# Performance work log

Measured on AMD Instinct MI355X. Metric: run time of the kernel, lower is better.

Reference implementation:

```python
import jax, jax.numpy as jnp
import numpy as np
from jax import lax

S, B, V, D, H, L, C = 2048, 32, 50000, 512, 512, 2, 10


def setup_inputs() -> dict:
    key = jax.random.key(0)
    ks = jax.random.split(key, 6)
    x = jax.random.randint(ks[0], (S, B), 0, V)  # (seq, batch) token ids
    embed = jax.random.normal(ks[1], (V, D), jnp.float32) * 0.1
    # per layer: W maps input -> [x_tilde, f_gate, r_gate], each H wide
    W = jax.random.normal(ks[2], (L, D, 3 * H), jnp.float32) * (1.0 / np.sqrt(D))
    b = jnp.zeros((L, 2 * H), jnp.float32)  # biases for f and r gates
    Wc = jax.random.normal(ks[3], (H, C), jnp.float32) * 0.05
    bc = jnp.zeros((C,), jnp.float32)
    return {"x": x, "embed": embed, "W": W, "b": b, "Wc": Wc, "bc": bc}


def _sru_layer(h_in, W_l, b_l):
    # h_in: (S, B, H) (input dim == hidden dim -> identity highway skip)
    U = jnp.einsum('sbd,dk->sbk', h_in, W_l)  # (S, B, 3H)
    xt, fg, rg = jnp.split(U, 3, axis=-1)
    bf, br = jnp.split(b_l, 2)
    f = jax.nn.sigmoid(fg + bf)
    r = jax.nn.sigmoid(rg + br)

    def step(c, inp):
        f_t, xt_t = inp
        c = f_t * c + (1.0 - f_t) * xt_t  # elementwise light recurrence
        return c, c

    c0 = jnp.zeros((h_in.shape[1], f.shape[-1]), h_in.dtype)
    _, cs = lax.scan(step, c0, (f, xt))  # cs: (S, B, H)
    # highway output
    return r * jnp.tanh(cs) + (1.0 - r) * h_in


def reference(x, embed, W, b, Wc, bc):
    h = embed[x]  # (S, B, D); dropout layers are identity at inference
    for l in range(W.shape[0]):
        h = _sru_layer(h, W[l], b[l])
    out = jnp.tanh(h)            # (S, B, H)
    pooled = jnp.max(out, axis=0)  # max-pool over time -> (B, H)
    pooled = jnp.tanh(pooled)
    return pooled @ Wc + bc      # (B, C)
```

## Files before the change

kernel.cpp:

```cpp
#include <hip/hip_runtime.h>
#include <cmath>

#define S_LEN 2048
#define B_SZ 32
#define D_DIM 512
#define H_DIM 512
#define C_NUM 10
#define M_ROWS (S_LEN * B_SZ)
#define BH (B_SZ * H_DIM)
#define N_COLS (3 * H_DIM)

#define SC 1024
#define SCH 32
#define NSUB 32
#define CROWS (SC * B_SZ)

typedef __bf16 bf16_t;
typedef bf16_t bf16x8 __attribute__((ext_vector_type(8)));
typedef float f32x4 __attribute__((ext_vector_type(4)));
typedef unsigned short ushort_t;

__device__ __forceinline__ unsigned int f2bf(float f) {
  union { float f; unsigned int u; } a;
  a.f = f;
  unsigned int r = a.u + 0x7FFFu + ((a.u >> 16) & 1u);
  return r >> 16;
}
__device__ __forceinline__ unsigned int pack2bf(float lo, float hi) {
  return f2bf(lo) | (f2bf(hi) << 16);
}
__device__ __forceinline__ float bflo(unsigned int u) {
  union { unsigned int u; float f; } a; a.u = u << 16; return a.f;
}
__device__ __forceinline__ float bfhi(unsigned int u) {
  union { unsigned int u; float f; } a; a.u = u & 0xffff0000u; return a.f;
}
__device__ __forceinline__ float sigf(float x) {
  return 1.f / (1.f + __expf(-x));
}
__device__ __forceinline__ float tanh_fast(float c) {
  float e = __expf(2.f * c);
  return 1.f - 2.f / (e + 1.f);
}
__device__ __forceinline__ void load16_lds(const void* g, void* l) {
  __builtin_amdgcn_global_load_lds(
      (const __attribute__((address_space(1))) unsigned int*)g,
      (__attribute__((address_space(3))) unsigned int*)l, 16, 0, 0);
}


__global__ __launch_bounds__(256) void gather_kernel(const int* __restrict__ x,
                                                     const float* __restrict__ embed,
                                                     uint4* __restrict__ E4) {
  int i = blockIdx.x * blockDim.x + threadIdx.x;
  const int total = M_ROWS * 16;
  int stride = gridDim.x * blockDim.x;
  for (; i < total; i += stride) {
    int m = i >> 4;
    int kg = (i & 15) * 4;
    int tile = m >> 7, row = m & 127;
    int xm = x[m];
    const float4* src = (const float4*)(embed + (size_t)xm * 512 + kg * 8);
    float4 v[8];
#pragma unroll
    for (int j = 0; j < 8; j++) v[j] = src[j];
    uint4* dst = E4 + (size_t)tile * 8192 + row;
#pragma unroll
    for (int j = 0; j < 4; j++) {
      dst[(size_t)(kg + j) * 128] =
          make_uint4(pack2bf(v[2 * j].x, v[2 * j].y), pack2bf(v[2 * j].z, v[2 * j].w),
                     pack2bf(v[2 * j + 1].x, v[2 * j + 1].y),
                     pack2bf(v[2 * j + 1].z, v[2 * j + 1].w));
    }
  }
}

__global__ __launch_bounds__(256) void wt_kernel(const float* __restrict__ W,
                                                 ushort_t* __restrict__ Wt) {
  int e = blockIdx.x * blockDim.x + threadIdx.x;
  if (e >= 2 * 786432) return;
  int l = e / 786432;
  int t = e - l * 786432;
  int ntile = t >> 16;
  int rr = t & 65535;
  int kc = rr >> 10;
  int row = (rr >> 3) & 127;
  int kk = t & 7;
  int n = ntile * 128 + row;
  int k = kc * 8 + kk;
  Wt[e] = (ushort_t)f2bf(W[(size_t)l * D_DIM * N_COLS + (size_t)k * N_COLS + n]);
}

__global__ __launch_bounds__(256, 3) void sru_gemm_bf16(
    const ushort_t* __restrict__ At,
    int tile0,
    const ushort_t* __restrict__ Bt,
    ushort_t* __restrict__ xt_out, ushort_t* __restrict__ f_out,
    ushort_t* __restrict__ r_out) {
  __shared__ ushort_t As[2][4096];
  __shared__ ushort_t Bs[2][4096];
  const int t = threadIdx.x;
  const int wave = t >> 6, lane = t & 63;
  const int cpx = gridDim.x >> 3;
  const int swz = (blockIdx.x & 7) * cpx + (blockIdx.x >> 3);
  const int nb = swz % 12, mb = swz / 12;
  const int m0 = mb * 128, n0 = nb * 128;
  const int wm = wave & 1, wn = wave >> 1;
  const int lrow = lane >> 4, lcol = lane & 15;

  f32x4 acc[4][4];
#pragma unroll
  for (int i = 0; i < 4; i++)
#pragma unroll
    for (int j = 0; j < 4; j++) acc[i][j] = (f32x4){0.f, 0.f, 0.f, 0.f};

  const ushort_t* Ab = At + ((size_t)(tile0 + mb) << 16);
  const ushort_t* Bb = Bt + ((size_t)nb << 16);
  const int c0 = wave * 2;
  const int le = lane * 8;

#define STAGE(buf, k0)                                                      \
  do {                                                                      \
    load16_lds(Ab + (k0) * 128 + (c0 + 0) * 512 + le, &As[buf][(c0 + 0) * 512]); \
    load16_lds(Ab + (k0) * 128 + (c0 + 1) * 512 + le, &As[buf][(c0 + 1) * 512]); \
    load16_lds(Bb + (k0) * 128 + (c0 + 0) * 512 + le, &Bs[buf][(c0 + 0) * 512]); \
    load16_lds(Bb + (k0) * 128 + (c0 + 1) * 512 + le, &Bs[buf][(c0 + 1) * 512]); \
  } while (0)

  STAGE(0, 0);
  __syncthreads();
  int cur = 0;
  for (int step = 0; step < 16; ++step) {
    if (step + 1 < 16) STAGE(cur ^ 1, (step + 1) * 32);
    bf16x8 af[4], bfr[4];
#pragma unroll
    for (int mi = 0; mi < 4; mi++)
      af[mi] = *reinterpret_cast<const bf16x8*>(
          &As[cur][(lrow * 128 + wm * 64 + mi * 16 + lcol) * 8]);
#pragma unroll
    for (int ni = 0; ni < 4; ni++)
      bfr[ni] = *reinterpret_cast<const bf16x8*>(
          &Bs[cur][(lrow * 128 + wn * 64 + ni * 16 + lcol) * 8]);
#pragma unroll
    for (int mi = 0; mi < 4; mi++)
#pragma unroll
      for (int ni = 0; ni < 4; ni++)
        acc[mi][ni] = __builtin_amdgcn_mfma_f32_16x16x32_bf16(
            bfr[ni], af[mi], acc[mi][ni], 0, 0, 0);
    __syncthreads();
    cur ^= 1;
  }
#undef STAGE

  const int region = n0 >> 9;
  ushort_t* outp = region == 0 ? xt_out : (region == 1 ? f_out : r_out);
  const int nloc0 = (n0 & 511) + wn * 64 + lrow * 4;
#pragma unroll
  for (int mi = 0; mi < 4; mi++) {
    const int m = m0 + wm * 64 + mi * 16 + lcol;
    const size_t mpart = ((size_t)(m >> 7) << 16) + ((size_t)(m & 127) << 3);
#pragma unroll
    for (int ni = 0; ni < 4; ni++) {
      const int nloc = nloc0 + ni * 16;
      size_t ad = mpart + ((size_t)(nloc >> 3) << 10) + (nloc & 7);
      uint2 pk;
      pk.x = pack2bf(acc[mi][ni][0], acc[mi][ni][1]);
      pk.y = pack2bf(acc[mi][ni][2], acc[mi][ni][3]);
      *(uint2*)&outp[ad] = pk;
    }
  }
}

template <int LAST>
__global__ __launch_bounds__(256) void scan_fused(
    const ushort_t* __restrict__ f, const ushort_t* __restrict__ xt,
    const ushort_t* __restrict__ r, const ushort_t* __restrict__ hw,
    ushort_t* __restrict__ ob, const float* __restrict__ bl,
    float* __restrict__ cstate, float* __restrict__ pmax,
    int first, int m0abs) {
  __shared__ float sA[8][32][8];
  __shared__ float sB[8][32][8];
  __shared__ float sC[8][32][8];
  const int tid = threadIdx.x;
  const int q = tid & 7, ch = tid >> 3;
  const int p = blockIdx.x * 8 + q;
  const int hc = p >> 5, b = p & 31;
  const int h0 = hc << 3;
  float bf_[8];
#pragma unroll
  for (int j = 0; j < 8; j++) bf_[j] = bl[h0 + j];

  {
    float Aa[8], Bv[8];
#pragma unroll
    for (int j = 0; j < 8; j++) { Aa[j] = 1.f; Bv[j] = 0.f; }
    for (int s = 0; s < SCH; s++) {
      int ml = ((ch * SCH + s) << 5) + b;
      size_t ga = ((size_t)(ml >> 7) << 16) + ((size_t)hc << 10) + ((ml & 127) << 3);
      uint4 fq = *(const uint4*)&f[ga];
      uint4 xq = *(const uint4*)&xt[ga];
      unsigned int fw[4] = {fq.x, fq.y, fq.z, fq.w};
      unsigned int xw[4] = {xq.x, xq.y, xq.z, xq.w};
#pragma unroll
      for (int w = 0; w < 4; w++) {
        float fa = sigf(bflo(fw[w]) + bf_[2 * w]);
        float fb = sigf(bfhi(fw[w]) + bf_[2 * w + 1]);
        Bv[2 * w]     = fa * Bv[2 * w]     + (1.f - fa) * bflo(xw[w]);
        Bv[2 * w + 1] = fb * Bv[2 * w + 1] + (1.f - fb) * bfhi(xw[w]);
        Aa[2 * w] *= fa;
        Aa[2 * w + 1] *= fb;
      }
    }
#pragma unroll
    for (int j = 0; j < 8; j++) { sA[j][ch][q] = Aa[j]; sB[j][ch][q] = Bv[j]; }
  }
  __syncthreads();

  if (tid < 64) {
    int qq = tid & 7, jj = tid >> 3;
    int pp = blockIdx.x * 8 + qq;
    int bb = pp & 31, hh = (pp >> 5) * 8 + jj;
    float c = first ? 0.f : cstate[bb * 512 + hh];
    float a_[NSUB], b_[NSUB];
#pragma unroll
    for (int cc = 0; cc < NSUB; cc++) { a_[cc] = sA[jj][cc][qq]; b_[cc] = sB[jj][cc][qq]; }
#pragma unroll
    for (int cc = 0; cc < NSUB; cc++) {
      sC[jj][cc][qq] = c;
      c = a_[cc] * c + b_[cc];
    }
    cstate[bb * 512 + hh] = c;
  }
  __syncthreads();

  float br_[8];
#pragma unroll
  for (int j = 0; j < 8; j++) br_[j] = bl[512 + h0 + j];
  float c[8], pm[8];
#pragma unroll
  for (int j = 0; j < 8; j++) { c[j] = sC[j][ch][q]; pm[j] = -1e30f; }
  for (int s = 0; s < SCH; s++) {
    int ml = ((ch * SCH + s) << 5) + b;
    size_t ga = ((size_t)(ml >> 7) << 16) + ((size_t)hc << 10) + ((ml & 127) << 3);
    int ma = m0abs + ml;
    size_t ha = ((size_t)(ma >> 7) << 16) + ((size_t)hc << 10) + ((ma & 127) << 3);
    uint4 fq = *(const uint4*)&f[ga];
    uint4 xq = *(const uint4*)&xt[ga];
    uint4 rq = *(const uint4*)&r[ga];
    uint4 hq = *(const uint4*)&hw[ha];
    unsigned int fw[4] = {fq.x, fq.y, fq.z, fq.w};
    unsigned int xw[4] = {xq.x, xq.y, xq.z, xq.w};
    unsigned int rw[4] = {rq.x, rq.y, rq.z, rq.w};
    unsigned int hv[4] = {hq.x, hq.y, hq.z, hq.w};
    unsigned int ow[4];
#pragma unroll
    for (int w = 0; w < 4; w++) {
      float fa = sigf(bflo(fw[w]) + bf_[2 * w]);
      float fb = sigf(bfhi(fw[w]) + bf_[2 * w + 1]);
      float ra = sigf(bflo(rw[w]) + br_[2 * w]);
      float rb = sigf(bfhi(rw[w]) + br_[2 * w + 1]);
      c[2 * w]     = fa * c[2 * w]     + (1.f - fa) * bflo(xw[w]);
      c[2 * w + 1] = fb * c[2 * w + 1] + (1.f - fb) * bfhi(xw[w]);
      float oa = ra * tanh_fast(c[2 * w]) + (1.f - ra) * bflo(hv[w]);
      float obv = rb * tanh_fast(c[2 * w + 1]) + (1.f - rb) * bfhi(hv[w]);
      if (LAST) {
        pm[2 * w] = fmaxf(pm[2 * w], oa);
        pm[2 * w + 1] = fmaxf(pm[2 * w + 1], obv);
      } else {
        ow[w] = pack2bf(oa, obv);
      }
    }
    if (!LAST) *(uint4*)&ob[ha] = make_uint4(ow[0], ow[1], ow[2], ow[3]);
  }
  if (LAST) {
    int lin = ch * BH + b * 512 + h0;
    if (first) {
#pragma unroll
      for (int j = 0; j < 8; j++) pmax[lin + j] = pm[j];
    } else {
#pragma unroll
      for (int j = 0; j < 8; j++) pmax[lin + j] = fmaxf(pmax[lin + j], pm[j]);
    }
  }
}

__global__ void pool_kernel(const float* __restrict__ pmax, float* __restrict__ pooled) {
  int rem = blockIdx.x * blockDim.x + threadIdx.x;
  float m = -1e30f;
  for (int ch = 0; ch < NSUB; ch++) m = fmaxf(m, pmax[ch * BH + rem]);
  pooled[rem] = tanhf(tanhf(m));
}

__global__ void out_gemm(const float* __restrict__ pooled, const float* __restrict__ Wc,
                         const float* __restrict__ bc, float* __restrict__ out) {
  __shared__ float pt[H_DIM];
  int b = blockIdx.x;
  for (int i = threadIdx.x; i < H_DIM; i += blockDim.x) pt[i] = pooled[b * H_DIM + i];
  __syncthreads();
  if (threadIdx.x < C_NUM) {
    int c = threadIdx.x;
    float acc = bc[c];
    for (int hh = 0; hh < H_DIM; hh++) acc = fmaf(pt[hh], Wc[hh * C_NUM + c], acc);
    out[b * C_NUM + c] = acc;
  }
}

extern "C" void kernel_launch(void* const* d_in, const int* in_sizes, int n_in,
                              void* d_out, int out_size, void* d_ws, size_t ws_size,
                              hipStream_t stream) {
  const int* x = (const int*)d_in[0];
  const float* embed = (const float*)d_in[1];
  const float* W = (const float*)d_in[2];
  const float* b = (const float*)d_in[3];
  const float* Wc = (const float*)d_in[4];
  const float* bc = (const float*)d_in[5];
  float* out = (float*)d_out;

  const size_t SZ_HB = (size_t)M_ROWS * H_DIM * 2;
  const size_t SZ_G  = (size_t)CROWS * H_DIM * 2;
  const size_t SZ_WT = 2ull * N_COLS * D_DIM * 2;
  const size_t SZ_BHf = (size_t)BH * 4;

  char* p = (char*)d_ws;
  float* cstate0 = (float*)p; p += SZ_BHf;
  float* cstate1 = (float*)p; p += SZ_BHf;
  float* pooled  = (float*)p; p += SZ_BHf;
  float* pmax    = (float*)p; p += (size_t)NSUB * SZ_BHf;
  ushort_t* Wt   = (ushort_t*)p; p += SZ_WT;
  ushort_t* E    = (ushort_t*)p; p += SZ_HB;
  ushort_t* OB   = (ushort_t*)p; p += SZ_HB;
  ushort_t* X0   = (ushort_t*)p; p += SZ_G;
  ushort_t* F0   = (ushort_t*)p; p += SZ_G;
  ushort_t* R0   = (ushort_t*)p;

  gather_kernel<<<4096, 256, 0, stream>>>(x, embed, (uint4*)E);
  wt_kernel<<<6144, 256, 0, stream>>>(W, Wt);

  const int gemm_blocks = (CROWS / 128) * (N_COLS / 128);
  const int NOUTER = S_LEN / SC;
  const float* bl0 = b;
  const float* bl1 = b + 2 * H_DIM;
  const ushort_t* Wt0 = Wt;
  const ushort_t* Wt1 = Wt + (size_t)N_COLS * D_DIM;

  for (int ci = 0; ci < NOUTER; ci++) {
    const int m0abs = ci * CROWS;
    const int tile0 = m0abs >> 7;
    sru_gemm_bf16<<<gemm_blocks, 256, 0, stream>>>(E, tile0, Wt0, X0, F0, R0);
    scan_fused<0><<<256, 256, 0, stream>>>(F0, X0, R0, E, OB, bl0, cstate0,
                                           nullptr, ci == 0, m0abs);
    sru_gemm_bf16<<<gemm_blocks, 256, 0, stream>>>(OB, tile0, Wt1, X0, F0, R0);
    scan_fused<1><<<256, 256, 0, stream>>>(F0, X0, R0, OB, nullptr, bl1, cstate1,
                                           pmax, ci == 0, m0abs);
  }

  pool_kernel<<<BH / 256, 256, 0, stream>>>(pmax, pooled);
  out_gemm<<<B_SZ, 256, 0, stream>>>(pooled, Wc, bc, out);
}
```

Baseline: 577.9 us.

## Triple-buffer GEMM LDS pipeline and widen scan to 1024-thread blocks

```diff
diff --git a/kernel.cpp b/kernel.cpp
--- a/kernel.cpp
+++ b/kernel.cpp
@@ -11,8 +11,8 @@
 #define N_COLS (3 * H_DIM)
 
 #define SC 1024
-#define SCH 32
-#define NSUB 32
+#define SCH 8
+#define NSUB 128
 #define CROWS (SC * B_SZ)
 
 typedef __bf16 bf16_t;
@@ -97,8 +97,8 @@
     const ushort_t* __restrict__ Bt,
     ushort_t* __restrict__ xt_out, ushort_t* __restrict__ f_out,
     ushort_t* __restrict__ r_out) {
-  __shared__ ushort_t As[2][4096];
-  __shared__ ushort_t Bs[2][4096];
+  __shared__ ushort_t As[3][4096];
+  __shared__ ushort_t Bs[3][4096];
   const int t = threadIdx.x;
   const int wave = t >> 6, lane = t & 63;
   const int cpx = gridDim.x >> 3;
@@ -128,10 +128,17 @@
   } while (0)
 
   STAGE(0, 0);
-  __syncthreads();
-  int cur = 0;
+  STAGE(1, 32);
+#pragma unroll
   for (int step = 0; step < 16; ++step) {
-    if (step + 1 < 16) STAGE(cur ^ 1, (step + 1) * 32);
+    if (step < 15)
+      asm volatile("s_waitcnt vmcnt(4)" ::: "memory");
+    else
+      asm volatile("s_waitcnt vmcnt(0)" ::: "memory");
+    __builtin_amdgcn_s_barrier();
+    asm volatile("" ::: "memory");
+    if (step < 14) STAGE((step + 2) % 3, (step + 2) * 32);
+    const int cur = step % 3;
     bf16x8 af[4], bfr[4];
 #pragma unroll
     for (int mi = 0; mi < 4; mi++)
@@ -147,8 +154,6 @@
       for (int ni = 0; ni < 4; ni++)
         acc[mi][ni] = __builtin_amdgcn_mfma_f32_16x16x32_bf16(
             bfr[ni], af[mi], acc[mi][ni], 0, 0, 0);
-    __syncthreads();
-    cur ^= 1;
   }
 #undef STAGE
 
@@ -172,15 +177,14 @@
 }
 
 template <int LAST>
-__global__ __launch_bounds__(256) void scan_fused(
+__global__ __launch_bounds__(1024) void scan_fused(
     const ushort_t* __restrict__ f, const ushort_t* __restrict__ xt,
     const ushort_t* __restrict__ r, const ushort_t* __restrict__ hw,
     ushort_t* __restrict__ ob, const float* __restrict__ bl,
     float* __restrict__ cstate, float* __restrict__ pmax,
     int first, int m0abs) {
-  __shared__ float sA[8][32][8];
-  __shared__ float sB[8][32][8];
-  __shared__ float sC[8][32][8];
+  __shared__ float sA[8][NSUB][8];
+  __shared__ float sB[8][NSUB][8];
   const int tid = threadIdx.x;
   const int q = tid & 7, ch = tid >> 3;
   const int p = blockIdx.x * 8 + q;
@@ -221,13 +225,11 @@
     int pp = blockIdx.x * 8 + qq;
     int bb = pp & 31, hh = (pp >> 5) * 8 + jj;
     float c = first ? 0.f : cstate[bb * 512 + hh];
-    float a_[NSUB], b_[NSUB];
-#pragma unroll
-    for (int cc = 0; cc < NSUB; cc++) { a_[cc] = sA[jj][cc][qq]; b_[cc] = sB[jj][cc][qq]; }
-#pragma unroll
     for (int cc = 0; cc < NSUB; cc++) {
-      sC[jj][cc][qq] = c;
-      c = a_[cc] * c + b_[cc];
+      float a = sA[jj][cc][qq];
+      float bv = sB[jj][cc][qq];
+      sA[jj][cc][qq] = c;
+      c = a * c + bv;
     }
     cstate[bb * 512 + hh] = c;
   }
@@ -238,7 +240,7 @@
   for (int j = 0; j < 8; j++) br_[j] = bl[512 + h0 + j];
   float c[8], pm[8];
 #pragma unroll
-  for (int j = 0; j < 8; j++) { c[j] = sC[j][ch][q]; pm[j] = -1e30f; }
+  for (int j = 0; j < 8; j++) { c[j] = sA[j][ch][q]; pm[j] = -1e30f; }
   for (int s = 0; s < SCH; s++) {
     int ml = ((ch * SCH + s) << 5) + b;
     size_t ga = ((size_t)(ml >> 7) << 16) + ((size_t)hc << 10) + ((ml & 127) << 3);
@@ -347,11 +349,11 @@
     const int m0abs = ci * CROWS;
     const int tile0 = m0abs >> 7;
     sru_gemm_bf16<<<gemm_blocks, 256, 0, stream>>>(E, tile0, Wt0, X0, F0, R0);
-    scan_fused<0><<<256, 256, 0, stream>>>(F0, X0, R0, E, OB, bl0, cstate0,
-                                           nullptr, ci == 0, m0abs);
+    scan_fused<0><<<256, 1024, 0, stream>>>(F0, X0, R0, E, OB, bl0, cstate0,
+                                            nullptr, ci == 0, m0abs);
     sru_gemm_bf16<<<gemm_blocks, 256, 0, stream>>>(OB, tile0, Wt1, X0, F0, R0);
-    scan_fused<1><<<256, 256, 0, stream>>>(F0, X0, R0, OB, nullptr, bl1, cstate1,
-                                           pmax, ci == 0, m0abs);
+    scan_fused<1><<<256, 1024, 0, stream>>>(F0, X0, R0, OB, nullptr, bl1, cstate1,
+                                            pmax, ci == 0, m0abs);
   }
 
   pool_kernel<<<BH / 256, 256, 0, stream>>>(pmax, pooled);
```

Measured after the change: 537.9 us. -6.9%, faster.
